# Optimization experiments

Measured on AMD Instinct MI355X. Metric: run time of the kernel, lower is better.

The kernel has to match this reference:

```python
import jax, jax.numpy as jnp
import numpy as np

H = 32        # query heads
KV = 8        # key/value heads
D = 128       # head_dim
GROUPS = H // KV
THETA = 10000.0


def _rope_cos_sin(position_ids):
    # position_ids: [B, S] int
    inv_freq = 1.0 / (THETA ** (jnp.arange(0, D, 2, dtype=jnp.float32) / D))  # [D/2]
    freqs = position_ids.astype(jnp.float32)[:, :, None] * inv_freq[None, None, :]  # [B,S,D/2]
    emb = jnp.concatenate([freqs, freqs], axis=-1)  # [B,S,D]
    return jnp.cos(emb), jnp.sin(emb)


def _rotate_half(x):
    x1, x2 = jnp.split(x, 2, axis=-1)
    return jnp.concatenate([-x2, x1], axis=-1)


def _apply_rope(x, cos, sin):
    # x: [B,h,S,D]; cos/sin: [B,S,D] -> broadcast over heads
    return x * cos[:, None, :, :] + _rotate_half(x) * sin[:, None, :, :]


def setup_inputs() -> dict:
    key = jax.random.key(0)
    ks = jax.random.split(key, 8)
    B, S, Dm = 2, 2048, 4096
    scale = lambda d: 1.0 / np.sqrt(d)
    hidden_states = jax.random.normal(ks[0], (B, S, Dm), dtype=jnp.float32)
    position_ids = jnp.broadcast_to(jnp.arange(S, dtype=jnp.int32)[None, :], (B, S))
    Wq = jax.random.normal(ks[1], (Dm, H * D), dtype=jnp.float32) * scale(Dm)
    Wk = jax.random.normal(ks[2], (Dm, KV * D), dtype=jnp.float32) * scale(Dm)
    Wv = jax.random.normal(ks[3], (Dm, KV * D), dtype=jnp.float32) * scale(Dm)
    Wo = jax.random.normal(ks[4], (H * D, Dm), dtype=jnp.float32) * scale(H * D)
    # per-head shift-encoder correction weights (small init so it's a correction)
    Ws_q = jax.random.normal(ks[5], (H, D, D), dtype=jnp.float32) * (0.02 * scale(D))
    Ws_k = jax.random.normal(ks[6], (H, D, D), dtype=jnp.float32) * (0.02 * scale(D))
    return {"hidden_states": hidden_states, "position_ids": position_ids,
            "Wq": Wq, "Wk": Wk, "Wv": Wv, "Wo": Wo, "Ws_q": Ws_q, "Ws_k": Ws_k}


def reference(hidden_states, position_ids, Wq, Wk, Wv, Wo, Ws_q, Ws_k):
    B, S, Dm = hidden_states.shape
    # projections -> [B, heads, S, D]
    q = (hidden_states @ Wq).reshape(B, S, H, D).transpose(0, 2, 1, 3)
    k = (hidden_states @ Wk).reshape(B, S, KV, D).transpose(0, 2, 1, 3)
    v = (hidden_states @ Wv).reshape(B, S, KV, D).transpose(0, 2, 1, 3)
    # RoPE
    cos, sin = _rope_cos_sin(position_ids)
    q = _apply_rope(q, cos, sin)
    k = _apply_rope(k, cos, sin)
    # GQA repeat_kv: [B,KV,S,D] -> [B,H,S,D]
    k = jnp.repeat(k, GROUPS, axis=1)
    v = jnp.repeat(v, GROUPS, axis=1)
    # causal SDPA
    scores = jnp.einsum('bhqd,bhkd->bhqk', q, k) / jnp.sqrt(jnp.float32(D))
    causal = jnp.tril(jnp.ones((S, S), dtype=bool))
    scores = jnp.where(causal[None, None, :, :], scores, jnp.float32(-1e30))
    probs = jax.nn.softmax(scores, axis=-1)
    attn = jnp.einsum('bhqk,bhkd->bhqd', probs, v)  # [B,H,S,D]
    attn = attn.transpose(0, 2, 1, 3)               # [B,S,H,D]
    # shift_encoder.do_shift: per-head linear correction from rotated Q and K
    delta = jnp.einsum('bhsd,hde->bshe', q, Ws_q) + jnp.einsum('bhsd,hde->bshe', k, Ws_k)
    attn = attn + delta
    # output projection
    out = attn.reshape(B, S, H * D) @ Wo
    return out
```

## Files before the change

kernel.cpp:

```cpp
#include <hip/hip_runtime.h>
#include <cstdint>

#define DEV __device__ __forceinline__

typedef __attribute__((ext_vector_type(4))) float  f32x4;
typedef __attribute__((ext_vector_type(8))) short  s16x8;
typedef __attribute__((ext_vector_type(4))) unsigned short u16x4;
typedef __attribute__((ext_vector_type(8))) unsigned short u16x8;

constexpr int B_   = 2;
constexpr int S_   = 2048;
constexpr int DM   = 4096;
constexpr int HQ   = 32;
constexpr int KVH  = 8;
constexpr int DH   = 128;
constexpr int NQKV = 6144;

DEV unsigned short f2bf(float f) {
  union { float f; unsigned u; } c; c.f = f;
  unsigned u = c.u + 0x7FFFu + ((c.u >> 16) & 1u);
  return (unsigned short)(u >> 16);
}
DEV float bf2f(unsigned short h) {
  union { unsigned u; float f; } c; c.u = (unsigned)h << 16; return c.f;
}
DEV void gload16(const void* g, const void* l) {
  __builtin_amdgcn_global_load_lds(
      (const __attribute__((address_space(1))) unsigned int*)(uintptr_t)g,
      (__attribute__((address_space(3))) unsigned int*)(unsigned)(uintptr_t)l,
      16, 0, 0);
}
DEV f32x4 mfma16x16(s16x8 a, s16x8 b, f32x4 c) {
  return __builtin_amdgcn_mfma_f32_16x16x32_bf16(a, b, c, 0, 0, 0);
}

__global__ __launch_bounds__(256) void k_tables(const int* __restrict__ pos,
                                                float* __restrict__ ct,
                                                float* __restrict__ st) {
  int i = blockIdx.x * 256 + threadIdx.x;
  if (i >= B_ * S_ * 64) return;
  int f = i & 63, bs = i >> 6;
  float p   = (float)pos[bs];
  float inv = __builtin_amdgcn_exp2f(-(float)f * 0.20762050593048355f);
  float a   = p * inv;
  ct[i] = cosf(a);
  st[i] = sinf(a);
}

__global__ __launch_bounds__(256) void k_cvt(const float* __restrict__ in,
                                             unsigned short* __restrict__ out,
                                             int n8) {
  int i = blockIdx.x * 256 + threadIdx.x;
  if (i >= n8) return;
  const f32x4* p = (const f32x4*)in + (size_t)2 * i;
  f32x4 a = p[0], b = p[1];
  u16x8 o;
  o[0] = f2bf(a[0]); o[1] = f2bf(a[1]); o[2] = f2bf(a[2]); o[3] = f2bf(a[3]);
  o[4] = f2bf(b[0]); o[5] = f2bf(b[1]); o[6] = f2bf(b[2]); o[7] = f2bf(b[3]);
  ((u16x8*)out)[i] = o;
}

__global__ __launch_bounds__(256) void k_tconv(const float* __restrict__ in,
                                               unsigned short* __restrict__ out,
                                               int R, int C,
                                               unsigned long long ibs,
                                               unsigned long long obs) {
  __shared__ float t[64][65];
  const int r0 = blockIdx.y * 64, c0 = blockIdx.x * 64;
  const float* ib = in + (size_t)blockIdx.z * ibs;
  unsigned short* ob = out + (size_t)blockIdx.z * obs;
  const int tid = threadIdx.x, tr = tid >> 4, c4 = (tid & 15) * 4;
#pragma unroll
  for (int it = 0; it < 4; ++it) {
    int rr = it * 16 + tr;
    f32x4 v = *(const f32x4*)&ib[(size_t)(r0 + rr) * C + (c0 + c4)];
    t[rr][c4 + 0] = v[0]; t[rr][c4 + 1] = v[1];
    t[rr][c4 + 2] = v[2]; t[rr][c4 + 3] = v[3];
  }
  __syncthreads();
#pragma unroll
  for (int it = 0; it < 4; ++it) {
    int cc = it * 16 + tr;
    u16x4 o;
    o[0] = f2bf(t[c4 + 0][cc]); o[1] = f2bf(t[c4 + 1][cc]);
    o[2] = f2bf(t[c4 + 2][cc]); o[3] = f2bf(t[c4 + 3][cc]);
    *(u16x4*)&ob[(size_t)(c0 + cc) * R + (r0 + c4)] = o;
  }
}

template <int BF16OUT>
__global__ __launch_bounds__(512, 2) void k_gemmN128(const unsigned short* __restrict__ A,
                                                     const unsigned short* __restrict__ BT,
                                                     void* __restrict__ Cv,
                                                     int M, int N, int K, int NBX) {
  extern __shared__ __align__(16) char L[];
  const int tid = threadIdx.x;
  const int lane = tid & 63, w = tid >> 6;
  const int g = lane >> 4, ml = lane & 15;
  const int wr = w & 1, wc = w >> 1;

  const int cpx = (int)gridDim.x >> 3;
  const int swz = ((int)blockIdx.x & 7) * cpx + ((int)blockIdx.x >> 3);
  const int by = swz / NBX, bx = swz - by * NBX;
  const int bm = by * 256, bn = bx * 128;

  const int srow_l = tid >> 3;
  const int scol_e = (((tid & 7) ^ ((tid >> 3) & 7)) << 3);
  const int nk = K >> 6;

#define STAGE(kt, hf) do {                                                        \
    if ((kt) < nk) {                                                              \
      const unsigned short* sb; char* db;                                         \
      if ((hf) < 2) { sb = A + (size_t)(bm + (hf) * 128) * K;                     \
                      db = L + ((kt) & 1) * 49152 + (hf) * 16384; }               \
      else          { sb = BT + (size_t)bn * K;                                   \
                      db = L + ((kt) & 1) * 49152 + 32768; }                      \
      sb += (size_t)(kt) * 64 + scol_e;                                           \
      _Pragma("unroll")                                                           \
      for (int r_ = 0; r_ < 2; ++r_)                                              \
        gload16(sb + (size_t)(r_ * 64 + srow_l) * K, db + r_ * 8192 + w * 1024);  \
    } } while (0)

  f32x4 Z = {0.f, 0.f, 0.f, 0.f};
  f32x4 acc[8][2];
#pragma unroll
  for (int i = 0; i < 8; ++i) { acc[i][0] = Z; acc[i][1] = Z; }
  s16x8 afr[4][2], bfr[2][2];

#define FRAG(base, row, ks)                                                       \
  ((const s16x8*)((base) + ((((row) >> 7) * 16384 + ((row) & 127) * 128 +         \
                             ((ks) * 32 + 8 * g) * 2) ^ (((row) & 7) << 4))))

#define PHASE(q, kbuf, SK1, H1, SK2, H2, VM) do {                                 \
    if ((q) == 0) {                                                               \
      _Pragma("unroll")                                                           \
      for (int nf = 0; nf < 2; ++nf)                                              \
        _Pragma("unroll")                                                         \
        for (int ks = 0; ks < 2; ++ks)                                            \
          bfr[nf][ks] = *FRAG(L + (kbuf) * 49152 + 32768,                         \
                              wc * 32 + nf * 16 + ml, ks);                        \
    }                                                                             \
    _Pragma("unroll")                                                             \
    for (int mm = 0; mm < 4; ++mm)                                                \
      _Pragma("unroll")                                                           \
      for (int ks = 0; ks < 2; ++ks)                                              \
        afr[mm][ks] = *FRAG(L + (kbuf) * 49152,                                   \
                            32 * (4 * (q) + mm) + 16 * wr + ml, ks);              \
    STAGE(SK1, H1);                                                               \
    if ((H2) >= 0) STAGE(SK2, H2);                                                \
    if ((VM) == 0) { asm volatile("s_waitcnt vmcnt(6)" ::: "memory"); }           \
    else if ((VM) == 1) {                                                         \
      if (last) { asm volatile("s_waitcnt vmcnt(2)" ::: "memory"); }              \
      else      { asm volatile("s_waitcnt vmcnt(6)" ::: "memory"); }              \
    } else if ((VM) == 2) {                                                       \
      if (last) { asm volatile("s_waitcnt vmcnt(0)" ::: "memory"); }              \
      else      { asm volatile("s_waitcnt vmcnt(6)" ::: "memory"); }              \
    } else {                                                                      \
      if (!last) { asm volatile("s_waitcnt vmcnt(6)" ::: "memory"); }             \
    }                                                                             \
    __builtin_amdgcn_s_barrier();                                                 \
    asm volatile("s_waitcnt lgkmcnt(0)" ::: "memory");                            \
    __builtin_amdgcn_sched_barrier(0);                                            \
    __builtin_amdgcn_s_setprio(1);                                                \
    _Pragma("unroll")                                                             \
    for (int mm = 0; mm < 4; ++mm)                                                \
      _Pragma("unroll")                                                           \
      for (int nf = 0; nf < 2; ++nf)                                              \
        _Pragma("unroll")                                                         \
        for (int ks = 0; ks < 2; ++ks)                                            \
          acc[4 * (q) + mm][nf] =                                                 \
              mfma16x16(afr[mm][ks], bfr[nf][ks], acc[4 * (q) + mm][nf]);         \
    __builtin_amdgcn_s_setprio(0);                                                \
    __builtin_amdgcn_s_barrier();                                                 \
  } while (0)

  STAGE(0, 0); STAGE(0, 1); STAGE(0, 2);
  STAGE(1, 0); STAGE(1, 2);
  asm volatile("s_waitcnt vmcnt(4)" ::: "memory");
  __builtin_amdgcn_s_barrier();

  const int iters = nk >> 1;
  for (int i = 0; i < iters; ++i) {
    const int t = 2 * i;
    const bool last = (i == iters - 1);
    PHASE(0, 0, t + 1, 1, -1, -1, 0);
    PHASE(1, 0, t + 2, 0, t + 2, 2, 1);
    PHASE(0, 1, t + 2, 1, -1, -1, 2);
    PHASE(1, 1, t + 3, 0, t + 3, 2, 3);
  }
#undef PHASE
#undef FRAG
#undef STAGE

  const int row0 = bm + 16 * wr + 4 * g, col0 = bn + wc * 32 + ml;
#pragma unroll
  for (int m = 0; m < 8; ++m)
#pragma unroll
    for (int nf = 0; nf < 2; ++nf)
#pragma unroll
      for (int r = 0; r < 4; ++r) {
        int row = row0 + 32 * m + r;
        int col = col0 + nf * 16;
        if (BF16OUT)
          ((unsigned short*)Cv)[(size_t)row * N + col] = f2bf(acc[m][nf][r]);
        else
          ((float*)Cv)[(size_t)row * N + col] = acc[m][nf][r];
      }
}

__global__ __launch_bounds__(256) void k_rope(const unsigned short* __restrict__ qkv,
                                              const float* __restrict__ ct,
                                              const float* __restrict__ st,
                                              unsigned short* __restrict__ qr,
                                              unsigned short* __restrict__ kr) {
  const int bs = blockIdx.x;
  const int b = bs >> 11, s = bs & 2047;
  const int tid = threadIdx.x;
  const float* cr = ct + (size_t)bs * 64;
  const float* sr = st + (size_t)bs * 64;
  const unsigned short* row = qkv + (size_t)bs * NQKV;
  {
    int h = tid >> 3, d0 = (tid & 7) * 16;
    u16x8 xs  = *(const u16x8*)&row[h * 128 + d0];
    u16x8 xs2 = *(const u16x8*)&row[h * 128 + d0 + 8];
    u16x8 xp  = *(const u16x8*)&row[h * 128 + (d0 ^ 64)];
    u16x8 xp2 = *(const u16x8*)&row[h * 128 + (d0 ^ 64) + 8];
    float sg = (d0 < 64) ? -1.f : 1.f;
    int ci = d0 & 63;
    u16x8 o1, o2;
#pragma unroll
    for (int j = 0; j < 8; ++j)
      o1[j] = f2bf(bf2f(xs[j]) * cr[ci + j] + sg * bf2f(xp[j]) * sr[ci + j]);
#pragma unroll
    for (int j = 0; j < 8; ++j)
      o2[j] = f2bf(bf2f(xs2[j]) * cr[ci + 8 + j] + sg * bf2f(xp2[j]) * sr[ci + 8 + j]);
    unsigned short* dst = qr + ((size_t)(b * HQ + h) * S_ + s) * DH + d0;
    *(u16x8*)dst = o1;
    *(u16x8*)(dst + 8) = o2;
  }
  if (tid < 64) {
    int kv = tid >> 3, d0 = (tid & 7) * 16;
    const unsigned short* krow = row + HQ * DH + kv * 128;
    u16x8 xs  = *(const u16x8*)&krow[d0];
    u16x8 xs2 = *(const u16x8*)&krow[d0 + 8];
    u16x8 xp  = *(const u16x8*)&krow[d0 ^ 64];
    u16x8 xp2 = *(const u16x8*)&krow[(d0 ^ 64) + 8];
    float sg = (d0 < 64) ? -1.f : 1.f;
    int ci = d0 & 63;
    u16x8 o1, o2;
#pragma unroll
    for (int j = 0; j < 8; ++j)
      o1[j] = f2bf(bf2f(xs[j]) * cr[ci + j] + sg * bf2f(xp[j]) * sr[ci + j]);
#pragma unroll
    for (int j = 0; j < 8; ++j)
      o2[j] = f2bf(bf2f(xs2[j]) * cr[ci + 8 + j] + sg * bf2f(xp2[j]) * sr[ci + 8 + j]);
    unsigned short* dst = kr + ((size_t)(b * KVH + kv) * S_ + s) * DH + d0;
    *(u16x8*)dst = o1;
    *(u16x8*)(dst + 8) = o2;
  }
}

__global__ __launch_bounds__(256) void k_vtrans(const unsigned short* __restrict__ qkv,
                                                unsigned short* __restrict__ vt) {
  __shared__ unsigned short t[64][65];
  const int z = blockIdx.z, b = z >> 3, kv = z & 7;
  const int s0 = blockIdx.x * 64, d0 = blockIdx.y * 64;
  const int tid = threadIdx.x, tr = tid >> 4, c4 = (tid & 15) * 4;
  const unsigned short* src = qkv + (size_t)(b * S_) * NQKV + HQ * DH + KVH * DH + kv * 128;
#pragma unroll
  for (int it = 0; it < 4; ++it) {
    int s = it * 16 + tr;
    u16x4 v = *(const u16x4*)&src[(size_t)(s0 + s) * NQKV + d0 + c4];
    t[s][c4 + 0] = v[0]; t[s][c4 + 1] = v[1];
    t[s][c4 + 2] = v[2]; t[s][c4 + 3] = v[3];
  }
  __syncthreads();
  unsigned short* dst = vt + (size_t)(b * KVH + kv) * DH * S_;
#pragma unroll
  for (int it = 0; it < 4; ++it) {
    int d = it * 16 + tr;
    u16x4 o;
    o[0] = t[c4 + 0][d]; o[1] = t[c4 + 1][d];
    o[2] = t[c4 + 2][d]; o[3] = t[c4 + 3][d];
    *(u16x4*)&dst[(size_t)(d0 + d) * S_ + s0 + c4] = o;
  }
}

__global__ __launch_bounds__(256) void k_attn(const unsigned short* __restrict__ qr,
                                              const unsigned short* __restrict__ kr,
                                              const unsigned short* __restrict__ vt,
                                              const unsigned short* __restrict__ wsq,
                                              const unsigned short* __restrict__ wsk,
                                              unsigned short* __restrict__ att) {
  const int h = blockIdx.y, b = blockIdx.z, kvh = h >> 2;
  const int tid = threadIdx.x, lane = tid & 63, w = tid >> 6;
  const int g = lane >> 4, ml = lane & 15;

  __shared__ unsigned short kvbuf[16384];
  __shared__ unsigned short pbuf[4][32 * 72];
  unsigned short* kl = kvbuf;
  unsigned short* vl = kvbuf + 8192;

  const unsigned short* Kg = kr + (size_t)(b * KVH + kvh) * S_ * DH;
  const unsigned short* Vg = vt + (size_t)(b * KVH + kvh) * DH * S_;
  const float CS = 0.12751745f;
  f32x4 Z = {0.f, 0.f, 0.f, 0.f};

  for (int half = 0; half < 2; ++half) {
    const int qbx = half ? (15 - (int)blockIdx.x) : (int)blockIdx.x;
    const int qb0 = qbx * 128;
    const unsigned short* Qg = qr + ((size_t)(b * HQ + h) * S_ + qb0) * DH;

    __syncthreads();
#pragma unroll
    for (int it = 0; it < 8; ++it) {
      int c = w + 4 * it;
      int off = c * 1024 + lane * 16;
      int row = off >> 8;
      int sch = ((off >> 4) & 15) ^ (row & 7);
      gload16(Qg + (size_t)row * DH + sch * 8, (const char*)kvbuf + c * 1024);
    }
    __syncthreads();
    s16x8 qfr[2][4];
#pragma unroll
    for (int qf = 0; qf < 2; ++qf)
#pragma unroll
      for (int ds = 0; ds < 4; ++ds) {
        int row = 32 * w + 16 * qf + ml;
        int sch = (4 * ds + g) ^ (row & 7);
        qfr[qf][ds] = *(const s16x8*)((const char*)kvbuf + row * 256 + sch * 16);
      }

    float mstate[2] = {-3e30f, -3e30f};
    float lstate[2] = {0.f, 0.f};
    f32x4 oacc[2][8];
    s16x8 kfr[2][4];
#pragma unroll
    for (int i = 0; i < 2; ++i)
#pragma unroll
      for (int j = 0; j < 8; ++j) oacc[i][j] = Z;

    const int ntiles = (qb0 >> 6) + 2;

    for (int t = 0; t < ntiles; ++t) {
      const int kv0 = t * 64;
      __syncthreads();
#pragma unroll
      for (int it = 0; it < 4; ++it) {
        int c = w + 4 * it;
        int off = c * 1024 + lane * 16;
        int row = off >> 8;
        int sch = ((off >> 4) & 15) ^ (row & 7);
        gload16(Kg + (size_t)(kv0 + row) * DH + sch * 8, (const char*)kl + c * 1024);
      }
#pragma unroll
      for (int it = 0; it < 4; ++it) {
        int c = w + 4 * it;
        int off = c * 1024 + lane * 16;
        int row = off >> 7;
        int sch = ((off >> 4) & 7) ^ (row & 7);
        gload16(Vg + (size_t)row * S_ + kv0 + sch * 8, (const char*)vl + c * 1024);
      }
      __syncthreads();

      f32x4 sacc[4][2];
#pragma unroll
      for (int i = 0; i < 4; ++i) { sacc[i][0] = Z; sacc[i][1] = Z; }
#pragma unroll
      for (int ds = 0; ds < 4; ++ds) {
        s16x8 af[4];
#pragma unroll
        for (int kf = 0; kf < 4; ++kf) {
          int row = 16 * kf + ml;
          int sch = (4 * ds + g) ^ (row & 7);
          af[kf] = *(const s16x8*)((const char*)kl + row * 256 + sch * 16);
        }
#pragma unroll
        for (int kf = 0; kf < 4; ++kf)
#pragma unroll
          for (int qf = 0; qf < 2; ++qf)
            sacc[kf][qf] = mfma16x16(af[kf], qfr[qf][ds], sacc[kf][qf]);
      }

      {
        int rel = kv0 - qb0;
        if (rel == ((w >> 1) << 6)) {
#pragma unroll
          for (int qf = 0; qf < 2; ++qf)
#pragma unroll
            for (int ds = 0; ds < 4; ++ds) {
              int row = 32 * w + 16 * qf + ml - rel;
              int sch = (4 * ds + g) ^ (row & 7);
              kfr[qf][ds] = *(const s16x8*)((const char*)kl + row * 256 + sch * 16);
            }
        }
      }

      const int qg = qb0 + 32 * w + ml;
      const bool fullTile = (kv0 + 63 <= qb0 + 32 * w);
      float alpha[2];
#pragma unroll
      for (int qf = 0; qf < 2; ++qf) {
        int qq = qg + 16 * qf;
        float mx = -3e30f;
        if (fullTile) {
#pragma unroll
          for (int kf = 0; kf < 4; ++kf)
#pragma unroll
            for (int r = 0; r < 4; ++r) {
              float sv = sacc[kf][qf][r] * CS;
              sacc[kf][qf][r] = sv;
              mx = fmaxf(mx, sv);
            }
        } else {
#pragma unroll
          for (int kf = 0; kf < 4; ++kf)
#pragma unroll
            for (int r = 0; r < 4; ++r) {
              float sv = sacc[kf][qf][r] * CS;
              int kk = kv0 + 16 * kf + 4 * g + r;
              sv = (kk <= qq) ? sv : -3e30f;
              sacc[kf][qf][r] = sv;
              mx = fmaxf(mx, sv);
            }
        }
        mx = fmaxf(mx, __shfl_xor(mx, 16));
        mx = fmaxf(mx, __shfl_xor(mx, 32));
        float mn = fmaxf(mstate[qf], mx);
        alpha[qf] = __builtin_amdgcn_exp2f(mstate[qf] - mn);
        mstate[qf] = mn;
        float ls = 0.f;
#pragma unroll
        for (int kf = 0; kf < 4; ++kf) {
          u16x4 pk;
#pragma unroll
          for (int r = 0; r < 4; ++r) {
            float p = __builtin_amdgcn_exp2f(sacc[kf][qf][r] - mn);
            ls += p;
            pk[r] = f2bf(p);
          }
          *(u16x4*)&pbuf[w][(16 * qf + ml) * 72 + 16 * kf + 4 * g] = pk;
        }
        ls += __shfl_xor(ls, 16);
        ls += __shfl_xor(ls, 32);
        lstate[qf] = lstate[qf] * alpha[qf] + ls;
      }
#pragma unroll
      for (int mf = 0; mf < 2; ++mf)
#pragma unroll
        for (int r = 0; r < 4; ++r) {
          float a = __shfl(alpha[mf], (lane & 48) | (4 * g + r));
#pragma unroll
          for (int nf = 0; nf < 8; ++nf) oacc[mf][nf][r] *= a;
        }
#pragma unroll
      for (int ks = 0; ks < 2; ++ks) {
        s16x8 pa[2];
#pragma unroll
        for (int mf = 0; mf < 2; ++mf)
          pa[mf] = *(const s16x8*)&pbuf[w][(16 * mf + ml) * 72 + 32 * ks + 8 * g];
#pragma unroll
        for (int nf = 0; nf < 8; ++nf) {
          int row = 16 * nf + ml;
          int sch = (4 * ks + g) ^ (row & 7);
          s16x8 bv = *(const s16x8*)((const char*)vl + row * 128 + sch * 16);
#pragma unroll
          for (int mf = 0; mf < 2; ++mf)
            oacc[mf][nf] = mfma16x16(pa[mf], bv, oacc[mf][nf]);
        }
      }
    }

#pragma unroll
    for (int mf = 0; mf < 2; ++mf)
#pragma unroll
      for (int r = 0; r < 4; ++r) {
        float li = __shfl(lstate[mf], (lane & 48) | (4 * g + r));
        float inv = 1.0f / li;
#pragma unroll
        for (int nf = 0; nf < 8; ++nf) oacc[mf][nf][r] *= inv;
      }

#pragma unroll
    for (int pass = 0; pass < 2; ++pass) {
      const unsigned short* Wg =
          (pass == 0 ? wsq : wsk) + (size_t)h * DH * DH;
      __syncthreads();
#pragma unroll
      for (int it = 0; it < 8; ++it) {
        int c = w + 4 * it;
        int off = c * 1024 + lane * 16;
        int row = off >> 8;
        int sch = ((off >> 4) & 15) ^ (row & 7);
        gload16(Wg + (size_t)row * DH + sch * 8, (const char*)kvbuf + c * 1024);
      }
      __syncthreads();
#pragma unroll
      for (int nf = 0; nf < 8; ++nf) {
        s16x8 wf[4];
#pragma unroll
        for (int ds = 0; ds < 4; ++ds) {
          int row = 16 * nf + ml;
          int sch = (4 * ds + g) ^ (row & 7);
          wf[ds] = *(const s16x8*)((const char*)kvbuf + row * 256 + sch * 16);
        }
#pragma unroll
        for (int qf = 0; qf < 2; ++qf)
#pragma unroll
          for (int ds = 0; ds < 4; ++ds)
            oacc[qf][nf] = mfma16x16(pass == 0 ? qfr[qf][ds] : kfr[qf][ds],
                                     wf[ds], oacc[qf][nf]);
      }
    }

#pragma unroll
    for (int mf = 0; mf < 2; ++mf)
#pragma unroll
      for (int r = 0; r < 4; ++r) {
        int rowg = b * S_ + qb0 + 32 * w + 16 * mf + 4 * g + r;
        size_t base = (size_t)rowg * (HQ * DH) + h * DH;
#pragma unroll
        for (int nf = 0; nf < 8; ++nf)
          att[base + 16 * nf + ml] = f2bf(oacc[mf][nf][r]);
      }
  }
}

extern "C" void kernel_launch(void* const* d_in, const int* in_sizes, int n_in,
                              void* d_out, int out_size, void* d_ws, size_t ws_size,
                              hipStream_t stream) {
  const float* hidden = (const float*)d_in[0];
  const int*   pos    = (const int*)d_in[1];
  const float* Wq     = (const float*)d_in[2];
  const float* Wk     = (const float*)d_in[3];
  const float* Wv     = (const float*)d_in[4];
  const float* Wo     = (const float*)d_in[5];
  const float* Wsq    = (const float*)d_in[6];
  const float* Wsk    = (const float*)d_in[7];

  char* ws = (char*)d_ws;
  unsigned short* XB    = (unsigned short*)(ws + 0);
  unsigned short* WQKVT = (unsigned short*)(ws + 33554432);
  unsigned short* WOT   = (unsigned short*)(ws + 83886080);
  unsigned short* WSQT  = (unsigned short*)(ws + 117440512);
  unsigned short* WSKT  = (unsigned short*)(ws + 118489088);
  float*          CT    = (float*)(ws + 119537664);
  float*          ST    = (float*)(ws + 120586240);
  unsigned short* QKV   = (unsigned short*)(ws + 121634816);
  unsigned short* QR    = (unsigned short*)(ws + 171966464);
  unsigned short* KR    = (unsigned short*)(ws + 205520896);
  unsigned short* VT    = (unsigned short*)(ws + 213909504);
  unsigned short* ATT   = (unsigned short*)(ws + 222298112);

  k_tables<<<1024, 256, 0, stream>>>(pos, CT, ST);
  k_cvt<<<8192, 256, 0, stream>>>(hidden, XB, 2097152);
  k_tconv<<<dim3(64, 64, 1), 256, 0, stream>>>(Wq, WQKVT, 4096, 4096, 0, 0);
  k_tconv<<<dim3(16, 64, 1), 256, 0, stream>>>(Wk, WQKVT + (size_t)4096 * 4096, 4096, 1024, 0, 0);
  k_tconv<<<dim3(16, 64, 1), 256, 0, stream>>>(Wv, WQKVT + (size_t)5120 * 4096, 4096, 1024, 0, 0);
  k_tconv<<<dim3(64, 64, 1), 256, 0, stream>>>(Wo, WOT, 4096, 4096, 0, 0);
  k_tconv<<<dim3(2, 2, 32), 256, 0, stream>>>(Wsq, WSQT, 128, 128, 16384, 16384);
  k_tconv<<<dim3(2, 2, 32), 256, 0, stream>>>(Wsk, WSKT, 128, 128, 16384, 16384);
  k_gemmN128<1><<<dim3(768), 512, 98304, stream>>>(XB, WQKVT, QKV, 4096, 6144, 4096, 48);
  k_rope<<<4096, 256, 0, stream>>>(QKV, CT, ST, QR, KR);
  k_vtrans<<<dim3(32, 2, 16), 256, 0, stream>>>(QKV, VT);
  k_attn<<<dim3(8, 32, 2), 256, 0, stream>>>(QR, KR, VT, WSQT, WSKT, ATT);
  k_gemmN128<0><<<dim3(512), 512, 98304, stream>>>(ATT, WOT, d_out, 4096, 4096, 4096, 32);
}
```

Baseline: 647.5 us.

## Enlarge GEMM tiles to 256x256 with reworked double-buffered pipeline

Changes the projection GEMM from 256x128 to 256x256 block tiles, so each warp computes a 32x64 output region per phase. The LDS layout, staging schedule, waitcnt pattern and phase sequence are rewritten for four A/B halves per k-step, and the last iteration is peeled. This raises arithmetic intensity per loaded byte and halves the number of blocks. In exchange it needs 128KB of LDS and more accumulator registers, which with 512 threads likely limits occupancy to one block per CU and leaves fewer blocks for the 256-CU device (256 blocks for the output GEMM).

```diff
diff --git a/kernel.cpp b/kernel.cpp
--- a/kernel.cpp
+++ b/kernel.cpp
@@ -89,10 +89,10 @@
 }
 
 template <int BF16OUT>
-__global__ __launch_bounds__(512, 2) void k_gemmN128(const unsigned short* __restrict__ A,
-                                                     const unsigned short* __restrict__ BT,
-                                                     void* __restrict__ Cv,
-                                                     int M, int N, int K, int NBX) {
+__global__ __launch_bounds__(512, 2) void k_gemm256(const unsigned short* __restrict__ A,
+                                                    const unsigned short* __restrict__ BT,
+                                                    void* __restrict__ Cv,
+                                                    int M, int N, int K, int NBX) {
   extern __shared__ __align__(16) char L[];
   const int tid = threadIdx.x;
   const int lane = tid & 63, w = tid >> 6;
@@ -102,7 +102,7 @@
   const int cpx = (int)gridDim.x >> 3;
   const int swz = ((int)blockIdx.x & 7) * cpx + ((int)blockIdx.x >> 3);
   const int by = swz / NBX, bx = swz - by * NBX;
-  const int bm = by * 256, bn = bx * 128;
+  const int bm = by * 256, bn = bx * 256;
 
   const int srow_l = tid >> 3;
   const int scol_e = (((tid & 7) ^ ((tid >> 3) & 7)) << 3);
@@ -111,10 +111,10 @@
 #define STAGE(kt, hf) do {                                                        \
     if ((kt) < nk) {                                                              \
       const unsigned short* sb; char* db;                                         \
-      if ((hf) < 2) { sb = A + (size_t)(bm + (hf) * 128) * K;                     \
-                      db = L + ((kt) & 1) * 49152 + (hf) * 16384; }               \
-      else          { sb = BT + (size_t)bn * K;                                   \
-                      db = L + ((kt) & 1) * 49152 + 32768; }                      \
+      if ((hf) < 2) { sb = A  + (size_t)(bm + (hf) * 128) * K;                    \
+                      db = L + ((kt) & 1) * 32768 + (hf) * 16384; }               \
+      else          { sb = BT + (size_t)(bn + ((hf) - 2) * 128) * K;              \
+                      db = L + 65536 + ((kt) & 1) * 32768 + ((hf) - 2) * 16384; } \
       sb += (size_t)(kt) * 64 + scol_e;                                           \
       _Pragma("unroll")                                                           \
       for (int r_ = 0; r_ < 2; ++r_)                                              \
@@ -122,81 +122,87 @@
     } } while (0)
 
   f32x4 Z = {0.f, 0.f, 0.f, 0.f};
-  f32x4 acc[8][2];
-#pragma unroll
-  for (int i = 0; i < 8; ++i) { acc[i][0] = Z; acc[i][1] = Z; }
-  s16x8 afr[4][2], bfr[2][2];
+  f32x4 acc[8][4];
+#pragma unroll
+  for (int i = 0; i < 8; ++i)
+#pragma unroll
+    for (int j = 0; j < 4; ++j) acc[i][j] = Z;
+  s16x8 bfr[4][2], afr[2][2];
 
 #define FRAG(base, row, ks)                                                       \
   ((const s16x8*)((base) + ((((row) >> 7) * 16384 + ((row) & 127) * 128 +         \
                              ((ks) * 32 + 8 * g) * 2) ^ (((row) & 7) << 4))))
 
-#define PHASE(q, kbuf, SK1, H1, SK2, H2, VM) do {                                 \
+#define PHASE(q, kbuf, SKT, SHF, VM) do {                                         \
     if ((q) == 0) {                                                               \
       _Pragma("unroll")                                                           \
-      for (int nf = 0; nf < 2; ++nf)                                              \
+      for (int nf = 0; nf < 4; ++nf)                                              \
         _Pragma("unroll")                                                         \
         for (int ks = 0; ks < 2; ++ks)                                            \
-          bfr[nf][ks] = *FRAG(L + (kbuf) * 49152 + 32768,                         \
-                              wc * 32 + nf * 16 + ml, ks);                        \
+          bfr[nf][ks] = *FRAG(L + 65536 + (kbuf) * 32768,                         \
+                              wc * 64 + nf * 16 + ml, ks);                        \
     }                                                                             \
     _Pragma("unroll")                                                             \
-    for (int mm = 0; mm < 4; ++mm)                                                \
+    for (int mm = 0; mm < 2; ++mm)                                                \
       _Pragma("unroll")                                                           \
       for (int ks = 0; ks < 2; ++ks)                                              \
-        afr[mm][ks] = *FRAG(L + (kbuf) * 49152,                                   \
-                            32 * (4 * (q) + mm) + 16 * wr + ml, ks);              \
-    STAGE(SK1, H1);                                                               \
-    if ((H2) >= 0) STAGE(SK2, H2);                                                \
-    if ((VM) == 0) { asm volatile("s_waitcnt vmcnt(6)" ::: "memory"); }           \
-    else if ((VM) == 1) {                                                         \
-      if (last) { asm volatile("s_waitcnt vmcnt(2)" ::: "memory"); }              \
-      else      { asm volatile("s_waitcnt vmcnt(6)" ::: "memory"); }              \
-    } else if ((VM) == 2) {                                                       \
-      if (last) { asm volatile("s_waitcnt vmcnt(0)" ::: "memory"); }              \
-      else      { asm volatile("s_waitcnt vmcnt(6)" ::: "memory"); }              \
-    } else {                                                                      \
-      if (!last) { asm volatile("s_waitcnt vmcnt(6)" ::: "memory"); }             \
-    }                                                                             \
+        afr[mm][ks] = *FRAG(L + (kbuf) * 32768,                                   \
+                            32 * (2 * (q) + mm) + 16 * wr + ml, ks);              \
+    STAGE(SKT, SHF);                                                              \
+    if ((VM) == 1) { asm volatile("s_waitcnt vmcnt(6)" ::: "memory"); }           \
+    else if ((VM) == 2) { asm volatile("s_waitcnt vmcnt(0)" ::: "memory"); }      \
     __builtin_amdgcn_s_barrier();                                                 \
     asm volatile("s_waitcnt lgkmcnt(0)" ::: "memory");                            \
-    __builtin_amdgcn_sched_barrier(0);                                            \
     __builtin_amdgcn_s_setprio(1);                                                \
     _Pragma("unroll")                                                             \
-    for (int mm = 0; mm < 4; ++mm)                                                \
+    for (int mm = 0; mm < 2; ++mm)                                                \
       _Pragma("unroll")                                                           \
-      for (int nf = 0; nf < 2; ++nf)                                              \
+      for (int nf = 0; nf < 4; ++nf)                                              \
         _Pragma("unroll")                                                         \
         for (int ks = 0; ks < 2; ++ks)                                            \
-          acc[4 * (q) + mm][nf] =                                                 \
-              mfma16x16(afr[mm][ks], bfr[nf][ks], acc[4 * (q) + mm][nf]);         \
+          acc[2 * (q) + mm][nf] =                                                 \
+              mfma16x16(afr[mm][ks], bfr[nf][ks], acc[2 * (q) + mm][nf]);         \
     __builtin_amdgcn_s_setprio(0);                                                \
     __builtin_amdgcn_s_barrier();                                                 \
   } while (0)
 
-  STAGE(0, 0); STAGE(0, 1); STAGE(0, 2);
-  STAGE(1, 0); STAGE(1, 2);
-  asm volatile("s_waitcnt vmcnt(4)" ::: "memory");
+  STAGE(0, 0); STAGE(0, 1); STAGE(0, 2); STAGE(0, 3);
+  STAGE(1, 2); STAGE(1, 3); STAGE(1, 0);
+  asm volatile("s_waitcnt vmcnt(6)" ::: "memory");
   __builtin_amdgcn_s_barrier();
 
   const int iters = nk >> 1;
-  for (int i = 0; i < iters; ++i) {
+  for (int i = 0; i < iters - 1; ++i) {
     const int t = 2 * i;
-    const bool last = (i == iters - 1);
-    PHASE(0, 0, t + 1, 1, -1, -1, 0);
-    PHASE(1, 0, t + 2, 0, t + 2, 2, 1);
-    PHASE(0, 1, t + 2, 1, -1, -1, 2);
-    PHASE(1, 1, t + 3, 0, t + 3, 2, 3);
+    PHASE(0, 0, t + 1, 1, 0);
+    PHASE(1, 0, t + 2, 2, 0);
+    PHASE(2, 0, t + 2, 0, 0);
+    PHASE(3, 0, t + 2, 3, 1);
+    PHASE(0, 1, t + 2, 1, 0);
+    PHASE(1, 1, t + 3, 2, 0);
+    PHASE(2, 1, t + 3, 3, 0);
+    PHASE(3, 1, t + 3, 0, 1);
+  }
+  {
+    const int t = nk - 2;
+    PHASE(0, 0, t + 1, 1, 0);
+    PHASE(1, 0, t + 2, 2, 0);
+    PHASE(2, 0, t + 2, 0, 0);
+    PHASE(3, 0, t + 2, 3, 2);
+    PHASE(0, 1, t + 2, 1, 0);
+    PHASE(1, 1, t + 3, 2, 0);
+    PHASE(2, 1, t + 3, 3, 0);
+    PHASE(3, 1, t + 3, 0, 0);
   }
 #undef PHASE
 #undef FRAG
 #undef STAGE
 
-  const int row0 = bm + 16 * wr + 4 * g, col0 = bn + wc * 32 + ml;
+  const int row0 = bm + 16 * wr + 4 * g, col0 = bn + wc * 64 + ml;
 #pragma unroll
   for (int m = 0; m < 8; ++m)
 #pragma unroll
-    for (int nf = 0; nf < 2; ++nf)
+    for (int nf = 0; nf < 4; ++nf)
 #pragma unroll
       for (int r = 0; r < 4; ++r) {
         int row = row0 + 32 * m + r;
@@ -560,9 +566,9 @@
   k_tconv<<<dim3(64, 64, 1), 256, 0, stream>>>(Wo, WOT, 4096, 4096, 0, 0);
   k_tconv<<<dim3(2, 2, 32), 256, 0, stream>>>(Wsq, WSQT, 128, 128, 16384, 16384);
   k_tconv<<<dim3(2, 2, 32), 256, 0, stream>>>(Wsk, WSKT, 128, 128, 16384, 16384);
-  k_gemmN128<1><<<dim3(768), 512, 98304, stream>>>(XB, WQKVT, QKV, 4096, 6144, 4096, 48);
+  k_gemm256<1><<<dim3(384), 512, 131072, stream>>>(XB, WQKVT, QKV, 4096, 6144, 4096, 24);
   k_rope<<<4096, 256, 0, stream>>>(QKV, CT, ST, QR, KR);
   k_vtrans<<<dim3(32, 2, 16), 256, 0, stream>>>(QKV, VT);
   k_attn<<<dim3(8, 32, 2), 256, 0, stream>>>(QR, KR, VT, WSQT, WSKT, ATT);
-  k_gemmN128<0><<<dim3(512), 512, 98304, stream>>>(ATT, WOT, d_out, 4096, 4096, 4096, 32);
-}
+  k_gemm256<0><<<dim3(256), 512, 131072, stream>>>(ATT, WOT, d_out, 4096, 4096, 4096, 16);
+}
```

Result: slower. 879.3 us (+35.8%).
